# Kernel tuning notes

Measured on AMD Instinct MI355X. Metric: run time of the kernel, lower is better.

## Reference

```python
import jax, jax.numpy as jnp
import numpy as np

B, S, F, H = 256, 512, 64, 128


def setup_inputs() -> dict:
    key = jax.random.key(0)
    ks = jax.random.split(key, 16)
    u = lambda k, shape, fan: jax.random.uniform(k, shape, jnp.float32, -1.0 / np.sqrt(fan), 1.0 / np.sqrt(fan))
    inp = {
        'x': jax.random.normal(ks[0], (B, S, F), jnp.float32),
        'm': (jax.random.uniform(ks[1], (B, S, F)) < 0.8).astype(jnp.float32),
        't': jax.random.uniform(ks[2], (B, S, F), jnp.float32),
        # temp_decay_h: Linear(F -> H)
        'Wdh': u(ks[3], (H, F), H), 'bdh': u(ks[4], (H,), H),
        # temp_decay_m: diagonal Linear(F -> F)
        'Wdm': u(ks[5], (F, F), F), 'bdm': u(ks[6], (F,), F),
        # time_reg: Linear(H -> F)
        'Wtr': u(ks[7], (F, H), H), 'btr': u(ks[8], (F,), H),
        # feat_reg: masked Linear(F -> F), zero diagonal
        'Wfr': u(ks[9], (F, F), F), 'bfr': u(ks[10], (F,), F),
        # weight_combine: Linear(2F -> F)
        'Wwc': u(ks[11], (F, 2 * F), 2 * F), 'bwc': u(ks[12], (F,), 2 * F),
        # LSTMCell(2F -> H)
        'Wih': u(ks[13], (4 * H, 2 * F), H), 'Whh': u(ks[14], (4 * H, H), H),
        'bih': u(ks[15], (4 * H,), H), 'bhh': u(jax.random.fold_in(key, 99), (4 * H,), H),
    }
    return inp


def _rits_forward(x, m, t, Wdh, bdh, Wdm, bdm, Wtr, btr, Wfr, bfr, Wwc, bwc, Wih, Whh, bih, bhh):
    f = x.shape[-1]
    hdim = Whh.shape[1]
    dWdm = jnp.diagonal(Wdm)                 # diag-masked temporal decay weight
    Wfr_m = Wfr * (1.0 - jnp.eye(f, dtype=Wfr.dtype))

    def step(carry, inputs):
        h, c, loss = carry
        xl, ml, tl = inputs                  # [B,F] each
        gamma_h = jnp.exp(-jax.nn.relu(tl @ Wdh.T + bdh))   # [B,H]
        gamma_m = jnp.exp(-jax.nn.relu(tl * dWdm + bdm))    # [B,F]
        h = h * gamma_h
        xl_hat = h @ Wtr.T + btr             # history-based estimate [B,F]
        denom = jnp.sum(ml) + 1e-5
        loss = loss + jnp.sum((xl - xl_hat) ** 2 * ml) / denom
        xl_c = ml * xl + (1.0 - ml) * xl_hat
        zl_hat = xl_c @ Wfr_m.T + bfr        # feature-based estimate
        loss = loss + jnp.sum((xl - zl_hat) ** 2 * ml) / denom
        beta = jnp.concatenate([gamma_m, ml], axis=1) @ Wwc.T + bwc
        cl_hat = beta * zl_hat + (1.0 - beta) * xl_hat
        loss = loss + jnp.sum((xl - cl_hat) ** 2 * ml) / denom
        cl_c = ml * xl + (1.0 - ml) * cl_hat
        inp = jnp.concatenate([cl_c, ml], axis=1)           # [B,2F]
        gates = inp @ Wih.T + bih + h @ Whh.T + bhh         # [B,4H]
        i, fg, g, o = jnp.split(gates, 4, axis=1)
        i, fg, o = jax.nn.sigmoid(i), jax.nn.sigmoid(fg), jax.nn.sigmoid(o)
        c = fg * c + i * jnp.tanh(g)
        h = o * jnp.tanh(c)
        return (h, c, loss), cl_c

    b, s, _ = x.shape
    h0 = jnp.zeros((b, hdim), x.dtype)
    c0 = jnp.zeros((b, hdim), x.dtype)
    xs = (jnp.swapaxes(x, 0, 1), jnp.swapaxes(m, 0, 1), jnp.swapaxes(t, 0, 1))
    (h, c, loss), imps = jax.lax.scan(step, (h0, c0, jnp.float32(0.0)), xs)
    imputations = jnp.swapaxes(imps, 0, 1)   # [B,S,F]
    return imputations, loss / s


def reference(x, m, t, Wdh, bdh, Wdm, bdm, Wtr, btr, Wfr, bfr, Wwc, bwc, Wih, Whh, bih, bhh):
    return _rits_forward(x, m, t, Wdh, bdh, Wdm, bdm, Wtr, btr, Wfr, bfr, Wwc, bwc, Wih, Whh, bih, bhh)
```

## Files before the change

### kernel.cpp

```cpp
#include <hip/hip_runtime.h>
#include <hip/hip_bf16.h>

#define Bsz 256
#define Ssz 512
#define Fsz 64
#define Hsz 128
#define NG  512

typedef unsigned short ushort_t;
typedef __attribute__((ext_vector_type(8))) short short8v;
typedef __attribute__((ext_vector_type(4))) float float4v;

__device__ __forceinline__ ushort_t f2bf(float f) {
  unsigned int b = __float_as_uint(f);
  return (ushort_t)((b + 0x7fffu + ((b >> 16) & 1u)) >> 16);
}

__global__ void denom_kernel(const float* __restrict__ m, float* __restrict__ inv_denom) {
  int s = blockIdx.x;
  int tid = threadIdx.x;
  const float4* mp = (const float4*)(m + ((size_t)tid * Ssz + s) * Fsz);
  float sum = 0.f;
#pragma unroll
  for (int i = 0; i < Fsz / 4; ++i) {
    float4 v = mp[i];
    sum += v.x + v.y + v.z + v.w;
  }
  for (int off = 32; off > 0; off >>= 1) sum += __shfl_xor(sum, off);
  __shared__ float red[4];
  if ((tid & 63) == 0) red[tid >> 6] = sum;
  __syncthreads();
  if (tid == 0) {
    float tot = red[0] + red[1] + red[2] + red[3];
    inv_denom[s] = 1.0f / (tot + 1e-5f);
  }
}

__global__ void pack_kernel(const float* __restrict__ Wih, const float* __restrict__ Whh,
                            ushort_t* __restrict__ Wpk) {
  int g = blockIdx.x * blockDim.x + threadIdx.x;
  if (g >= 16384) return;
  int lane = g & 63, nt = (g >> 6) & 31, kt = g >> 11;
  int jout = nt * 16 + (lane & 15);
  int kbase = kt * 32 + ((lane >> 4) << 3);
  ushort_t* dst = Wpk + (size_t)g * 8;
#pragma unroll
  for (int j = 0; j < 8; ++j) {
    int k = kbase + j;
    float w = (k < 128) ? Wih[jout * 128 + k] : Whh[jout * 128 + (k - 128)];
    dst[j] = f2bf(w);
  }
}

__launch_bounds__(512, 2)
__global__ void rits_kernel(
    const float* __restrict__ x, const float* __restrict__ m, const float* __restrict__ t,
    const float* __restrict__ Wdh, const float* __restrict__ bdh,
    const float* __restrict__ Wdm, const float* __restrict__ bdm,
    const float* __restrict__ Wtr, const float* __restrict__ btr,
    const float* __restrict__ Wfr, const float* __restrict__ bfr,
    const float* __restrict__ Wwc, const float* __restrict__ bwc,
    const float* __restrict__ bih, const float* __restrict__ bhh,
    const ushort_t* __restrict__ Wpk, const float* __restrict__ inv_denom,
    float* __restrict__ out_imp, float* __restrict__ out_loss)
{
  const int b = blockIdx.x;
  const int tid = threadIdx.x;
  const int lane = tid & 63;
  const int wv = tid >> 6;

  __shared__ float sWdh[Hsz][68];
  __shared__ float sWtr[Fsz][132];
  __shared__ float sWwc[Fsz][132];
  __shared__ float sWfr[Fsz][68];
  __shared__ float sbdh[Hsz], sdWdm[Fsz], sbdm[Fsz], sbtr[Fsz], sbfr[Fsz], sbwc[Fsz];
  __shared__ float sH[Hsz], sC[Hsz];
  __shared__ __align__(16) ushort_t sVh[256];
  __shared__ float sB2[128];
  __shared__ __align__(16) float sXl[Fsz], sMl[Fsz], sTl[Fsz];
  __shared__ float sXlhat[Fsz], sBeta[Fsz], sXlc[Fsz];
  __shared__ float sGates[NG];
  __shared__ float sRed[8];

  for (int i = tid; i < Hsz * Fsz; i += 512) sWdh[i >> 6][i & 63] = Wdh[i];
  for (int i = tid; i < Fsz * Hsz; i += 512) sWtr[i >> 7][i & 127] = Wtr[i];
  for (int i = tid; i < Fsz * Hsz; i += 512) sWwc[i >> 7][i & 127] = Wwc[i];
  for (int i = tid; i < Fsz * Fsz; i += 512) {
    int r = i >> 6, c = i & 63;
    sWfr[r][c] = (r == c) ? 0.f : Wfr[i];
  }
  if (tid < Hsz) { sbdh[tid] = bdh[tid]; sH[tid] = 0.f; sC[tid] = 0.f; }
  if (tid < Fsz) {
    sdWdm[tid] = Wdm[tid * Fsz + tid];
    sbdm[tid] = bdm[tid]; sbtr[tid] = btr[tid];
    sbfr[tid] = bfr[tid]; sbwc[tid] = bwc[tid];
  }

  const short8v* wp = (const short8v*)Wpk;
  short8v Bf[8][4];
#pragma unroll
  for (int kt = 0; kt < 8; ++kt)
#pragma unroll
    for (int n = 0; n < 4; ++n)
      Bf[kt][n] = wp[((kt * 32 + wv * 4 + n) << 6) + lane];
  float gb[4];
#pragma unroll
  for (int n = 0; n < 4; ++n) {
    int j = (wv * 4 + n) * 16 + (lane & 15);
    gb[n] = bih[j] + bhh[j];
  }

  const float* xp = x + (size_t)b * Ssz * Fsz;
  const float* mp = m + (size_t)b * Ssz * Fsz;
  const float* tp = t + (size_t)b * Ssz * Fsz;
  float* op = out_imp + (size_t)b * Ssz * Fsz;

  float4 pre;
  if (tid < 16)      pre = *(const float4*)(xp + tid * 4);
  else if (tid < 32) pre = *(const float4*)(mp + (tid - 16) * 4);
  else if (tid < 48) pre = *(const float4*)(tp + (tid - 32) * 4);
  if (tid < 16) {
    *(float4*)&sXl[tid * 4] = pre;
  } else if (tid < 32) {
    int i = tid - 16;
    *(float4*)&sMl[i * 4] = pre;
    *(float4*)&sB2[64 + i * 4] = pre;
    sVh[64 + i * 4 + 0] = f2bf(pre.x);
    sVh[64 + i * 4 + 1] = f2bf(pre.y);
    sVh[64 + i * 4 + 2] = f2bf(pre.z);
    sVh[64 + i * 4 + 3] = f2bf(pre.w);
  } else if (tid < 48) {
    *(float4*)&sTl[(tid - 32) * 4] = pre;
  }
  __syncthreads();

  float lacc = 0.f;

  for (int s = 0; s < Ssz; ++s) {
    const float idn = inv_denom[s];

    {
      int out = tid >> 2, p = tid & 3;
      float sum = 0.f;
#pragma unroll
      for (int i = 0; i < 16; ++i) {
        int k = p + 4 * i;
        sum += sWdh[out][k] * sTl[k];
      }
      sum += __shfl_xor(sum, 1);
      sum += __shfl_xor(sum, 2);
      if (p == 0) {
        float gh = __expf(-fmaxf(0.f, sum + sbdh[out]));
        float hv = sH[out] * gh;
        sH[out] = hv;
        sVh[128 + out] = f2bf(hv);
      }
      if (tid < Fsz) {
        float gm = __expf(-fmaxf(0.f, sTl[tid] * sdWdm[tid] + sbdm[tid]));
        sB2[tid] = gm;
      }
    }
    __syncthreads();

    if (tid < 256) {
      int out = tid >> 2, p = tid & 3;
      float sum = 0.f;
#pragma unroll
      for (int i = 0; i < 32; ++i) {
        int k = p + 4 * i;
        sum += sWtr[out][k] * sH[k];
      }
      sum += __shfl_xor(sum, 1);
      sum += __shfl_xor(sum, 2);
      if (p == 0) {
        float xlh = sum + sbtr[out];
        sXlhat[out] = xlh;
        float xv = sXl[out], mv = sMl[out];
        sXlc[out] = mv * xv + (1.f - mv) * xlh;
        float d = xv - xlh;
        lacc += d * d * mv * idn;
      }
    } else {
      int tt = tid - 256;
      int out = tt >> 2, p = tt & 3;
      float sum = 0.f;
#pragma unroll
      for (int i = 0; i < 32; ++i) {
        int k = p + 4 * i;
        sum += sWwc[out][k] * sB2[k];
      }
      sum += __shfl_xor(sum, 1);
      sum += __shfl_xor(sum, 2);
      if (p == 0) sBeta[out] = sum + sbwc[out];
    }
    __syncthreads();

    {
      int out = tid >> 3, p = tid & 7;
      float sum = 0.f;
#pragma unroll
      for (int i = 0; i < 8; ++i) {
        int k = p + 8 * i;
        sum += sWfr[out][k] * sXlc[k];
      }
      sum += __shfl_xor(sum, 1);
      sum += __shfl_xor(sum, 2);
      sum += __shfl_xor(sum, 4);
      if (p == 0) {
        float zl = sum + sbfr[out];
        float xv = sXl[out], mv = sMl[out];
        float xlh = sXlhat[out], beta = sBeta[out];
        float d2 = xv - zl;
        float clh = beta * zl + (1.f - beta) * xlh;
        float d3 = xv - clh;
        lacc += (d2 * d2 + d3 * d3) * mv * idn;
        float clc = mv * xv + (1.f - mv) * clh;
        sVh[out] = f2bf(clc);
        op[s * Fsz + out] = clc;
      }
    }
    __syncthreads();

    {
      int ps = (s + 1 < Ssz) ? s + 1 : Ssz - 1;
      if (tid < 16)      pre = *(const float4*)(xp + ps * Fsz + tid * 4);
      else if (tid < 32) pre = *(const float4*)(mp + ps * Fsz + (tid - 16) * 4);
      else if (tid < 48) pre = *(const float4*)(tp + ps * Fsz + (tid - 32) * 4);

      const char* abase = (const char*)sVh + ((lane >> 4) << 4);
      float4v acc[4];
#pragma unroll
      for (int n = 0; n < 4; ++n) acc[n] = (float4v){gb[n], gb[n], gb[n], gb[n]};
#pragma unroll
      for (int kt = 0; kt < 8; ++kt) {
        short8v a = *(const short8v*)(abase + kt * 64);
#pragma unroll
        for (int n = 0; n < 4; ++n)
          acc[n] = __builtin_amdgcn_mfma_f32_16x16x32_bf16(a, Bf[kt][n], acc[n], 0, 0, 0);
      }
      if (lane < 16) {
#pragma unroll
        for (int n = 0; n < 4; ++n)
          sGates[(wv * 4 + n) * 16 + lane] = acc[n][0];
      }
    }
    __syncthreads();

    if (tid < Hsz) {
      float gi = sGates[tid], gf = sGates[128 + tid], gg = sGates[256 + tid], go = sGates[384 + tid];
      float si = 1.f / (1.f + __expf(-gi));
      float sf = 1.f / (1.f + __expf(-gf));
      float so = 1.f / (1.f + __expf(-go));
      float c = sf * sC[tid] + si * tanhf(gg);
      sC[tid] = c;
      sH[tid] = so * tanhf(c);
    }
    if (tid < 16) {
      *(float4*)&sXl[tid * 4] = pre;
    } else if (tid < 32) {
      int i = tid - 16;
      *(float4*)&sMl[i * 4] = pre;
      *(float4*)&sB2[64 + i * 4] = pre;
      sVh[64 + i * 4 + 0] = f2bf(pre.x);
      sVh[64 + i * 4 + 1] = f2bf(pre.y);
      sVh[64 + i * 4 + 2] = f2bf(pre.z);
      sVh[64 + i * 4 + 3] = f2bf(pre.w);
    } else if (tid < 48) {
      *(float4*)&sTl[(tid - 32) * 4] = pre;
    }
    __syncthreads();
  }

  for (int off = 32; off > 0; off >>= 1) lacc += __shfl_xor(lacc, off);
  if ((tid & 63) == 0) sRed[tid >> 6] = lacc;
  __syncthreads();
  if (tid == 0) {
    float tot = 0.f;
#pragma unroll
    for (int w = 0; w < 8; ++w) tot += sRed[w];
    atomicAdd(out_loss, tot * (1.0f / Ssz));
  }
}

extern "C" void kernel_launch(void* const* d_in, const int* in_sizes, int n_in,
                              void* d_out, int out_size, void* d_ws, size_t ws_size,
                              hipStream_t stream) {
  const float* x   = (const float*)d_in[0];
  const float* m   = (const float*)d_in[1];
  const float* t   = (const float*)d_in[2];
  const float* Wdh = (const float*)d_in[3];
  const float* bdh = (const float*)d_in[4];
  const float* Wdm = (const float*)d_in[5];
  const float* bdm = (const float*)d_in[6];
  const float* Wtr = (const float*)d_in[7];
  const float* btr = (const float*)d_in[8];
  const float* Wfr = (const float*)d_in[9];
  const float* bfr = (const float*)d_in[10];
  const float* Wwc = (const float*)d_in[11];
  const float* bwc = (const float*)d_in[12];
  const float* Wih = (const float*)d_in[13];
  const float* Whh = (const float*)d_in[14];
  const float* bih = (const float*)d_in[15];
  const float* bhh = (const float*)d_in[16];

  float* inv_denom = (float*)d_ws;
  ushort_t* Wpk = (ushort_t*)((char*)d_ws + 2048);
  float* out_f = (float*)d_out;
  float* out_loss = out_f + (size_t)Bsz * Ssz * Fsz;

  denom_kernel<<<Ssz, 256, 0, stream>>>(m, inv_denom);
  pack_kernel<<<64, 256, 0, stream>>>(Wih, Whh, Wpk);
  hipMemsetAsync(out_loss, 0, sizeof(float), stream);
  rits_kernel<<<Bsz, 512, 0, stream>>>(x, m, t, Wdh, bdh, Wdm, bdm, Wtr, btr, Wfr, bfr,
                                       Wwc, bwc, bih, bhh, Wpk, inv_denom, out_f, out_loss);
}
```

Baseline: 1.629 ms.

## Precompute gamma_h and beta off the recurrence, shrink sequential step work

Moves the non-recurrent temporal decay projection and the beta weight-combine GEMM into separate batched MFMA kernels that write bf16 results to workspace. The recurrent kernel then loads those per-step values and keeps the Wtr and Wfr weights in registers, computing their products as split partial sums across waves. The LSTM MFMA over the h and mask part of the input is issued before the imputation chain so it overlaps, and fast sigmoid/tanh approximations replace tanhf. The cost is extra workspace traffic, bf16 rounding of gamma_h and beta, and the recurrent kernel dropping to one block per CU.

```diff
diff --git a/kernel.cpp b/kernel.cpp
--- a/kernel.cpp
+++ b/kernel.cpp
@@ -14,6 +14,14 @@
 __device__ __forceinline__ ushort_t f2bf(float f) {
   unsigned int b = __float_as_uint(f);
   return (ushort_t)((b + 0x7fffu + ((b >> 16) & 1u)) >> 16);
+}
+__device__ __forceinline__ float bf2f(ushort_t u) {
+  return __uint_as_float(((unsigned int)u) << 16);
+}
+__device__ __forceinline__ float sigf(float v) { return 1.f / (1.f + __expf(-v)); }
+__device__ __forceinline__ float tanhf_fast(float v) {
+  float e = __expf(2.f * v);
+  return 1.f - 2.f / (e + 1.f);
 }
 
 __global__ void denom_kernel(const float* __restrict__ m, float* __restrict__ inv_denom) {
@@ -52,16 +60,161 @@
   }
 }
 
-__launch_bounds__(512, 2)
+__global__ void gh_kernel(const float* __restrict__ t, const float* __restrict__ Wdh,
+                          const float* __restrict__ bdh, ushort_t* __restrict__ gh) {
+  const int tid = threadIdx.x;
+  const int lane = tid & 63, wv = tid >> 6;
+  const int row0 = blockIdx.x * 64;
+  __shared__ __align__(16) ushort_t st[64][72];
+  __shared__ __align__(16) ushort_t sO[64][136];
+  __shared__ float sbdh[128];
+  if (tid < 128) sbdh[tid] = bdh[tid];
+  short8v Bf[2][8];
+#pragma unroll
+  for (int kt = 0; kt < 2; ++kt)
+#pragma unroll
+    for (int nt = 0; nt < 8; ++nt) {
+      int col = nt * 16 + (lane & 15);
+      int k0 = kt * 32 + ((lane >> 4) << 3);
+      float4 wa = *(const float4*)(Wdh + col * 64 + k0);
+      float4 wb = *(const float4*)(Wdh + col * 64 + k0 + 4);
+      short8v bb;
+      bb[0] = (short)f2bf(wa.x); bb[1] = (short)f2bf(wa.y);
+      bb[2] = (short)f2bf(wa.z); bb[3] = (short)f2bf(wa.w);
+      bb[4] = (short)f2bf(wb.x); bb[5] = (short)f2bf(wb.y);
+      bb[6] = (short)f2bf(wb.z); bb[7] = (short)f2bf(wb.w);
+      Bf[kt][nt] = bb;
+    }
+  const float* tb = t + (size_t)row0 * 64;
+  {
+    int r = tid >> 2, c0 = (tid & 3) * 16;
+#pragma unroll
+    for (int q = 0; q < 4; ++q) {
+      float4 v = *(const float4*)(tb + r * 64 + c0 + q * 4);
+      st[r][c0 + q * 4 + 0] = f2bf(v.x);
+      st[r][c0 + q * 4 + 1] = f2bf(v.y);
+      st[r][c0 + q * 4 + 2] = f2bf(v.z);
+      st[r][c0 + q * 4 + 3] = f2bf(v.w);
+    }
+  }
+  __syncthreads();
+  float4v acc[8] = {};
+#pragma unroll
+  for (int kt = 0; kt < 2; ++kt) {
+    int r = wv * 16 + (lane & 15);
+    int k0 = kt * 32 + ((lane >> 4) << 3);
+    short8v a = *(const short8v*)&st[r][k0];
+#pragma unroll
+    for (int nt = 0; nt < 8; ++nt)
+      acc[nt] = __builtin_amdgcn_mfma_f32_16x16x32_bf16(a, Bf[kt][nt], acc[nt], 0, 0, 0);
+  }
+#pragma unroll
+  for (int nt = 0; nt < 8; ++nt)
+#pragma unroll
+    for (int rr = 0; rr < 4; ++rr) {
+      int col = nt * 16 + (lane & 15);
+      int row = wv * 16 + ((lane >> 4) << 2) + rr;
+      float v = acc[nt][rr] + sbdh[col];
+      sO[row][col] = f2bf(__expf(-fmaxf(0.f, v)));
+    }
+  __syncthreads();
+  {
+    int r = tid >> 2, c0 = (tid & 3) * 32;
+    const uint4* src = (const uint4*)&sO[r][c0];
+    uint4* dst = (uint4*)(gh + (size_t)(row0 + r) * 128 + c0);
+#pragma unroll
+    for (int q = 0; q < 4; ++q) dst[q] = src[q];
+  }
+}
+
+__global__ void beta_kernel(const float* __restrict__ t, const float* __restrict__ m,
+                            const float* __restrict__ Wdm, const float* __restrict__ bdm,
+                            const float* __restrict__ Wwc, const float* __restrict__ bwc,
+                            ushort_t* __restrict__ beta) {
+  const int tid = threadIdx.x;
+  const int lane = tid & 63, wv = tid >> 6;
+  const int row0 = blockIdx.x * 64;
+  __shared__ __align__(16) ushort_t sA[64][136];
+  __shared__ __align__(16) ushort_t sO[64][72];
+  __shared__ float sdw[64], sbd[64], sbwc[64];
+  if (tid < 64) {
+    sdw[tid] = Wdm[tid * 64 + tid];
+    sbd[tid] = bdm[tid];
+    sbwc[tid] = bwc[tid];
+  }
+  short8v Bf[4][4];
+#pragma unroll
+  for (int kt = 0; kt < 4; ++kt)
+#pragma unroll
+    for (int nt = 0; nt < 4; ++nt) {
+      int col = nt * 16 + (lane & 15);
+      int k0 = kt * 32 + ((lane >> 4) << 3);
+      float4 wa = *(const float4*)(Wwc + col * 128 + k0);
+      float4 wb = *(const float4*)(Wwc + col * 128 + k0 + 4);
+      short8v bb;
+      bb[0] = (short)f2bf(wa.x); bb[1] = (short)f2bf(wa.y);
+      bb[2] = (short)f2bf(wa.z); bb[3] = (short)f2bf(wa.w);
+      bb[4] = (short)f2bf(wb.x); bb[5] = (short)f2bf(wb.y);
+      bb[6] = (short)f2bf(wb.z); bb[7] = (short)f2bf(wb.w);
+      Bf[kt][nt] = bb;
+    }
+  __syncthreads();
+  {
+    int r = tid >> 2, c0 = (tid & 3) * 16;
+    const float* tb = t + (size_t)row0 * 64;
+    const float* mb = m + (size_t)row0 * 64;
+#pragma unroll
+    for (int q = 0; q < 4; ++q) {
+      float4 tv = *(const float4*)(tb + r * 64 + c0 + q * 4);
+      float4 mv = *(const float4*)(mb + r * 64 + c0 + q * 4);
+      int c = c0 + q * 4;
+      sA[r][c + 0] = f2bf(__expf(-fmaxf(0.f, tv.x * sdw[c + 0] + sbd[c + 0])));
+      sA[r][c + 1] = f2bf(__expf(-fmaxf(0.f, tv.y * sdw[c + 1] + sbd[c + 1])));
+      sA[r][c + 2] = f2bf(__expf(-fmaxf(0.f, tv.z * sdw[c + 2] + sbd[c + 2])));
+      sA[r][c + 3] = f2bf(__expf(-fmaxf(0.f, tv.w * sdw[c + 3] + sbd[c + 3])));
+      sA[r][64 + c + 0] = f2bf(mv.x);
+      sA[r][64 + c + 1] = f2bf(mv.y);
+      sA[r][64 + c + 2] = f2bf(mv.z);
+      sA[r][64 + c + 3] = f2bf(mv.w);
+    }
+  }
+  __syncthreads();
+  float4v acc[4] = {};
+#pragma unroll
+  for (int kt = 0; kt < 4; ++kt) {
+    int r = wv * 16 + (lane & 15);
+    int k0 = kt * 32 + ((lane >> 4) << 3);
+    short8v a = *(const short8v*)&sA[r][k0];
+#pragma unroll
+    for (int nt = 0; nt < 4; ++nt)
+      acc[nt] = __builtin_amdgcn_mfma_f32_16x16x32_bf16(a, Bf[kt][nt], acc[nt], 0, 0, 0);
+  }
+#pragma unroll
+  for (int nt = 0; nt < 4; ++nt)
+#pragma unroll
+    for (int rr = 0; rr < 4; ++rr) {
+      int col = nt * 16 + (lane & 15);
+      int row = wv * 16 + ((lane >> 4) << 2) + rr;
+      sO[row][col] = f2bf(acc[nt][rr] + sbwc[col]);
+    }
+  __syncthreads();
+  {
+    int r = tid >> 2, c0 = (tid & 3) * 16;
+    const uint4* src = (const uint4*)&sO[r][c0];
+    uint4* dst = (uint4*)(beta + (size_t)(row0 + r) * 64 + c0);
+    dst[0] = src[0];
+    dst[1] = src[1];
+  }
+}
+
+__launch_bounds__(512, 1)
 __global__ void rits_kernel(
-    const float* __restrict__ x, const float* __restrict__ m, const float* __restrict__ t,
-    const float* __restrict__ Wdh, const float* __restrict__ bdh,
-    const float* __restrict__ Wdm, const float* __restrict__ bdm,
+    const float* __restrict__ x, const float* __restrict__ m,
     const float* __restrict__ Wtr, const float* __restrict__ btr,
     const float* __restrict__ Wfr, const float* __restrict__ bfr,
-    const float* __restrict__ Wwc, const float* __restrict__ bwc,
     const float* __restrict__ bih, const float* __restrict__ bhh,
     const ushort_t* __restrict__ Wpk, const float* __restrict__ inv_denom,
+    const ushort_t* __restrict__ ghp, const ushort_t* __restrict__ betap,
     float* __restrict__ out_imp, float* __restrict__ out_loss)
 {
   const int b = blockIdx.x;
@@ -69,32 +222,40 @@
   const int lane = tid & 63;
   const int wv = tid >> 6;
 
-  __shared__ float sWdh[Hsz][68];
-  __shared__ float sWtr[Fsz][132];
-  __shared__ float sWwc[Fsz][132];
-  __shared__ float sWfr[Fsz][68];
-  __shared__ float sbdh[Hsz], sdWdm[Fsz], sbdm[Fsz], sbtr[Fsz], sbfr[Fsz], sbwc[Fsz];
-  __shared__ float sH[Hsz], sC[Hsz];
+  __shared__ float sIdn[Ssz];
+  __shared__ float sPart[8][64];
+  __shared__ float sPartF[8][64];
+  __shared__ float sGates[NG];
+  __shared__ float sH[Hsz];
   __shared__ __align__(16) ushort_t sVh[256];
-  __shared__ float sB2[128];
-  __shared__ __align__(16) float sXl[Fsz], sMl[Fsz], sTl[Fsz];
-  __shared__ float sXlhat[Fsz], sBeta[Fsz], sXlc[Fsz];
-  __shared__ float sGates[NG];
-  __shared__ float sRed[8];
-
-  for (int i = tid; i < Hsz * Fsz; i += 512) sWdh[i >> 6][i & 63] = Wdh[i];
-  for (int i = tid; i < Fsz * Hsz; i += 512) sWtr[i >> 7][i & 127] = Wtr[i];
-  for (int i = tid; i < Fsz * Hsz; i += 512) sWwc[i >> 7][i & 127] = Wwc[i];
-  for (int i = tid; i < Fsz * Fsz; i += 512) {
-    int r = i >> 6, c = i & 63;
-    sWfr[r][c] = (r == c) ? 0.f : Wfr[i];
-  }
-  if (tid < Hsz) { sbdh[tid] = bdh[tid]; sH[tid] = 0.f; sC[tid] = 0.f; }
-  if (tid < Fsz) {
-    sdWdm[tid] = Wdm[tid * Fsz + tid];
-    sbdm[tid] = bdm[tid]; sbtr[tid] = btr[tid];
-    sbfr[tid] = bfr[tid]; sbwc[tid] = bwc[tid];
-  }
+
+  sIdn[tid] = inv_denom[tid];
+
+  float wtr_r[16];
+  {
+    const float* wb = Wtr + lane * 128 + wv * 16;
+#pragma unroll
+    for (int q = 0; q < 4; ++q) {
+      float4 v = *(const float4*)(wb + q * 4);
+      wtr_r[q * 4 + 0] = v.x; wtr_r[q * 4 + 1] = v.y;
+      wtr_r[q * 4 + 2] = v.z; wtr_r[q * 4 + 3] = v.w;
+    }
+  }
+  float wfr_r[8];
+  {
+    const float* wb = Wfr + lane * 64 + wv * 8;
+#pragma unroll
+    for (int q = 0; q < 2; ++q) {
+      float4 v = *(const float4*)(wb + q * 4);
+      wfr_r[q * 4 + 0] = v.x; wfr_r[q * 4 + 1] = v.y;
+      wfr_r[q * 4 + 2] = v.z; wfr_r[q * 4 + 3] = v.w;
+    }
+#pragma unroll
+    for (int i = 0; i < 8; ++i)
+      if (lane == wv * 8 + i) wfr_r[i] = 0.f;
+  }
+  const float btr_r = btr[lane];
+  const float bfr_r = bfr[lane];
 
   const short8v* wp = (const short8v*)Wpk;
   short8v Bf[8][4];
@@ -112,132 +273,94 @@
 
   const float* xp = x + (size_t)b * Ssz * Fsz;
   const float* mp = m + (size_t)b * Ssz * Fsz;
-  const float* tp = t + (size_t)b * Ssz * Fsz;
+  const ushort_t* ghb = ghp + (size_t)b * Ssz * 128;
+  const ushort_t* beb = betap + (size_t)b * Ssz * 64;
   float* op = out_imp + (size_t)b * Ssz * Fsz;
 
-  float4 pre;
-  if (tid < 16)      pre = *(const float4*)(xp + tid * 4);
-  else if (tid < 32) pre = *(const float4*)(mp + (tid - 16) * 4);
-  else if (tid < 48) pre = *(const float4*)(tp + (tid - 32) * 4);
-  if (tid < 16) {
-    *(float4*)&sXl[tid * 4] = pre;
-  } else if (tid < 32) {
-    int i = tid - 16;
-    *(float4*)&sMl[i * 4] = pre;
-    *(float4*)&sB2[64 + i * 4] = pre;
-    sVh[64 + i * 4 + 0] = f2bf(pre.x);
-    sVh[64 + i * 4 + 1] = f2bf(pre.y);
-    sVh[64 + i * 4 + 2] = f2bf(pre.z);
-    sVh[64 + i * 4 + 3] = f2bf(pre.w);
-  } else if (tid < 48) {
-    *(float4*)&sTl[(tid - 32) * 4] = pre;
-  }
+  if (tid < Hsz) sH[tid] = 0.f;
+  if (tid < 128) sVh[128 + tid] = 0;
+  float c_reg = 0.f;
+
+  float xv_cur = xp[lane];
+  float mv_cur = mp[lane];
+  float bet_cur = bf2f(beb[lane]);
+  if (wv == 0) sVh[64 + lane] = f2bf(mv_cur);
   __syncthreads();
 
   float lacc = 0.f;
 
   for (int s = 0; s < Ssz; ++s) {
-    const float idn = inv_denom[s];
+    const int ps = (s + 1 < Ssz) ? s + 1 : Ssz - 1;
+    float xv_nxt = xp[ps * 64 + lane];
+    float mv_nxt = mp[ps * 64 + lane];
+    ushort_t bet_raw = beb[ps * 64 + lane];
+    ushort_t gh_raw = 0;
+    if (tid < 128) gh_raw = ghb[(size_t)ps * 128 + tid];
 
     {
-      int out = tid >> 2, p = tid & 3;
-      float sum = 0.f;
-#pragma unroll
-      for (int i = 0; i < 16; ++i) {
-        int k = p + 4 * i;
-        sum += sWdh[out][k] * sTl[k];
-      }
-      sum += __shfl_xor(sum, 1);
-      sum += __shfl_xor(sum, 2);
-      if (p == 0) {
-        float gh = __expf(-fmaxf(0.f, sum + sbdh[out]));
-        float hv = sH[out] * gh;
-        sH[out] = hv;
-        sVh[128 + out] = f2bf(hv);
-      }
-      if (tid < Fsz) {
-        float gm = __expf(-fmaxf(0.f, sTl[tid] * sdWdm[tid] + sbdm[tid]));
-        sB2[tid] = gm;
-      }
-    }
-    __syncthreads();
-
-    if (tid < 256) {
-      int out = tid >> 2, p = tid & 3;
-      float sum = 0.f;
-#pragma unroll
-      for (int i = 0; i < 32; ++i) {
-        int k = p + 4 * i;
-        sum += sWtr[out][k] * sH[k];
-      }
-      sum += __shfl_xor(sum, 1);
-      sum += __shfl_xor(sum, 2);
-      if (p == 0) {
-        float xlh = sum + sbtr[out];
-        sXlhat[out] = xlh;
-        float xv = sXl[out], mv = sMl[out];
-        sXlc[out] = mv * xv + (1.f - mv) * xlh;
-        float d = xv - xlh;
-        lacc += d * d * mv * idn;
-      }
-    } else {
-      int tt = tid - 256;
-      int out = tt >> 2, p = tt & 3;
-      float sum = 0.f;
-#pragma unroll
-      for (int i = 0; i < 32; ++i) {
-        int k = p + 4 * i;
-        sum += sWwc[out][k] * sB2[k];
-      }
-      sum += __shfl_xor(sum, 1);
-      sum += __shfl_xor(sum, 2);
-      if (p == 0) sBeta[out] = sum + sbwc[out];
-    }
-    __syncthreads();
-
+      const float4* h4 = (const float4*)&sH[wv * 16];
+      float4 h0 = h4[0], h1 = h4[1], h2 = h4[2], h3 = h4[3];
+      float part = wtr_r[0] * h0.x + wtr_r[1] * h0.y + wtr_r[2] * h0.z + wtr_r[3] * h0.w
+                 + wtr_r[4] * h1.x + wtr_r[5] * h1.y + wtr_r[6] * h1.z + wtr_r[7] * h1.w
+                 + wtr_r[8] * h2.x + wtr_r[9] * h2.y + wtr_r[10] * h2.z + wtr_r[11] * h2.w
+                 + wtr_r[12] * h3.x + wtr_r[13] * h3.y + wtr_r[14] * h3.z + wtr_r[15] * h3.w;
+      sPart[wv][lane] = part;
+    }
+
+    float4v acc[4];
+#pragma unroll
+    for (int n = 0; n < 4; ++n) acc[n] = (float4v){gb[n], gb[n], gb[n], gb[n]};
     {
-      int out = tid >> 3, p = tid & 7;
-      float sum = 0.f;
-#pragma unroll
-      for (int i = 0; i < 8; ++i) {
-        int k = p + 8 * i;
-        sum += sWfr[out][k] * sXlc[k];
-      }
-      sum += __shfl_xor(sum, 1);
-      sum += __shfl_xor(sum, 2);
-      sum += __shfl_xor(sum, 4);
-      if (p == 0) {
-        float zl = sum + sbfr[out];
-        float xv = sXl[out], mv = sMl[out];
-        float xlh = sXlhat[out], beta = sBeta[out];
-        float d2 = xv - zl;
-        float clh = beta * zl + (1.f - beta) * xlh;
-        float d3 = xv - clh;
-        lacc += (d2 * d2 + d3 * d3) * mv * idn;
-        float clc = mv * xv + (1.f - mv) * clh;
-        sVh[out] = f2bf(clc);
-        op[s * Fsz + out] = clc;
-      }
-    }
-    __syncthreads();
-
-    {
-      int ps = (s + 1 < Ssz) ? s + 1 : Ssz - 1;
-      if (tid < 16)      pre = *(const float4*)(xp + ps * Fsz + tid * 4);
-      else if (tid < 32) pre = *(const float4*)(mp + ps * Fsz + (tid - 16) * 4);
-      else if (tid < 48) pre = *(const float4*)(tp + ps * Fsz + (tid - 32) * 4);
-
       const char* abase = (const char*)sVh + ((lane >> 4) << 4);
-      float4v acc[4];
-#pragma unroll
-      for (int n = 0; n < 4; ++n) acc[n] = (float4v){gb[n], gb[n], gb[n], gb[n]};
-#pragma unroll
-      for (int kt = 0; kt < 8; ++kt) {
+#pragma unroll
+      for (int kt = 2; kt < 8; ++kt) {
         short8v a = *(const short8v*)(abase + kt * 64);
 #pragma unroll
         for (int n = 0; n < 4; ++n)
           acc[n] = __builtin_amdgcn_mfma_f32_16x16x32_bf16(a, Bf[kt][n], acc[n], 0, 0, 0);
       }
+    }
+    __syncthreads();
+
+    float xlh = btr_r;
+#pragma unroll
+    for (int w = 0; w < 8; ++w) xlh += sPart[w][lane];
+    const float xv = xv_cur, mv = mv_cur;
+    const float xlc = mv * xv + (1.f - mv) * xlh;
+    const float idn = sIdn[s];
+    if (wv == 0) { float d = xv - xlh; lacc += d * d * mv * idn; }
+    {
+      float pf = 0.f;
+#pragma unroll
+      for (int i = 0; i < 8; ++i) pf += wfr_r[i] * __shfl(xlc, wv * 8 + i);
+      sPartF[wv][lane] = pf;
+    }
+    __syncthreads();
+
+    float zl = bfr_r;
+#pragma unroll
+    for (int w = 0; w < 8; ++w) zl += sPartF[w][lane];
+    const float beta = bet_cur;
+    const float clh = beta * zl + (1.f - beta) * xlh;
+    const float clc = mv * xv + (1.f - mv) * clh;
+    if (wv == 0) {
+      float d2 = xv - zl, d3 = xv - clh;
+      lacc += (d2 * d2 + d3 * d3) * mv * idn;
+      op[s * 64 + lane] = clc;
+    }
+    {
+      const int kb = (lane >> 4) << 3;
+      short8v A0, A1;
+#pragma unroll
+      for (int j = 0; j < 8; ++j) {
+        A0[j] = (short)f2bf(__shfl(clc, kb + j));
+        A1[j] = (short)f2bf(__shfl(clc, 32 + kb + j));
+      }
+#pragma unroll
+      for (int n = 0; n < 4; ++n) {
+        acc[n] = __builtin_amdgcn_mfma_f32_16x16x32_bf16(A0, Bf[0][n], acc[n], 0, 0, 0);
+        acc[n] = __builtin_amdgcn_mfma_f32_16x16x32_bf16(A1, Bf[1][n], acc[n], 0, 0, 0);
+      }
       if (lane < 16) {
 #pragma unroll
         for (int n = 0; n < 4; ++n)
@@ -246,39 +369,27 @@
     }
     __syncthreads();
 
-    if (tid < Hsz) {
-      float gi = sGates[tid], gf = sGates[128 + tid], gg = sGates[256 + tid], go = sGates[384 + tid];
-      float si = 1.f / (1.f + __expf(-gi));
-      float sf = 1.f / (1.f + __expf(-gf));
-      float so = 1.f / (1.f + __expf(-go));
-      float c = sf * sC[tid] + si * tanhf(gg);
-      sC[tid] = c;
-      sH[tid] = so * tanhf(c);
-    }
-    if (tid < 16) {
-      *(float4*)&sXl[tid * 4] = pre;
-    } else if (tid < 32) {
-      int i = tid - 16;
-      *(float4*)&sMl[i * 4] = pre;
-      *(float4*)&sB2[64 + i * 4] = pre;
-      sVh[64 + i * 4 + 0] = f2bf(pre.x);
-      sVh[64 + i * 4 + 1] = f2bf(pre.y);
-      sVh[64 + i * 4 + 2] = f2bf(pre.z);
-      sVh[64 + i * 4 + 3] = f2bf(pre.w);
-    } else if (tid < 48) {
-      *(float4*)&sTl[(tid - 32) * 4] = pre;
-    }
+    if (tid < 128) {
+      float gi = sGates[tid], gf = sGates[128 + tid];
+      float gg = sGates[256 + tid], go = sGates[384 + tid];
+      float cc = sigf(gf) * c_reg + sigf(gi) * tanhf_fast(gg);
+      c_reg = cc;
+      float hn = sigf(go) * tanhf_fast(cc);
+      float hv = hn * bf2f(gh_raw);
+      sH[tid] = hv;
+      sVh[128 + tid] = f2bf(hv);
+    }
+    if (wv == 0) sVh[64 + lane] = f2bf(mv_nxt);
     __syncthreads();
-  }
-
-  for (int off = 32; off > 0; off >>= 1) lacc += __shfl_xor(lacc, off);
-  if ((tid & 63) == 0) sRed[tid >> 6] = lacc;
-  __syncthreads();
-  if (tid == 0) {
-    float tot = 0.f;
-#pragma unroll
-    for (int w = 0; w < 8; ++w) tot += sRed[w];
-    atomicAdd(out_loss, tot * (1.0f / Ssz));
+
+    xv_cur = xv_nxt;
+    mv_cur = mv_nxt;
+    bet_cur = bf2f(bet_raw);
+  }
+
+  if (wv == 0) {
+    for (int off = 32; off > 0; off >>= 1) lacc += __shfl_xor(lacc, off);
+    if (lane == 0) atomicAdd(out_loss, lacc * (1.0f / Ssz));
   }
 }
 
@@ -303,14 +414,19 @@
   const float* bih = (const float*)d_in[15];
   const float* bhh = (const float*)d_in[16];
 
-  float* inv_denom = (float*)d_ws;
-  ushort_t* Wpk = (ushort_t*)((char*)d_ws + 2048);
+  char* ws = (char*)d_ws;
+  float* inv_denom = (float*)ws;
+  ushort_t* Wpk    = (ushort_t*)(ws + 2048);
+  ushort_t* gh_ws  = (ushort_t*)(ws + 264192);
+  ushort_t* be_ws  = (ushort_t*)(ws + 264192 + (size_t)Bsz * Ssz * 128 * 2);
   float* out_f = (float*)d_out;
   float* out_loss = out_f + (size_t)Bsz * Ssz * Fsz;
 
   denom_kernel<<<Ssz, 256, 0, stream>>>(m, inv_denom);
   pack_kernel<<<64, 256, 0, stream>>>(Wih, Whh, Wpk);
+  gh_kernel<<<(Bsz * Ssz) / 64, 256, 0, stream>>>(t, Wdh, bdh, gh_ws);
+  beta_kernel<<<(Bsz * Ssz) / 64, 256, 0, stream>>>(t, m, Wdm, bdm, Wwc, bwc, be_ws);
   hipMemsetAsync(out_loss, 0, sizeof(float), stream);
-  rits_kernel<<<Bsz, 512, 0, stream>>>(x, m, t, Wdh, bdh, Wdm, bdm, Wtr, btr, Wfr, bfr,
-                                       Wwc, bwc, bih, bhh, Wpk, inv_denom, out_f, out_loss);
-}
+  rits_kernel<<<Bsz, 512, 0, stream>>>(x, m, Wtr, btr, Wfr, bfr, bih, bhh,
+                                       Wpk, inv_denom, gh_ws, be_ws, out_f, out_loss);
+}
```

Result: faster. 1.486 ms (-8.8%).
